# Kernel tuning notes

Hardware: AMD Instinct MI355X
Metric: run time of the kernel (lower is better)

## Reference

```python
import jax, jax.numpy as jnp
import numpy as np

N_NODES = 50000
N_EDGES = 1600000
NFEAT = 512
NCLASS = 16
H1, C1 = 8, 16  # conv1: heads=8, out_channels=16 (concat -> 128)
H2, C2 = 1, NCLASS  # conv2: heads=1, concat=False
NEG_SLOPE = 0.2


def gat_layer(x, edge_index, W, att_src, att_dst, bias, heads, out_c, concat):
    """PyG GATConv (eval mode, add_self_loops=True).
    x: [N, F_in]; edge_index: [2, E]; W: [heads*out_c, F_in];
    att_src/att_dst: [heads, out_c]; bias: [heads*out_c] or [out_c]."""
    N = x.shape[0]
    loop = jnp.arange(N, dtype=edge_index.dtype)
    src = jnp.concatenate([edge_index[0], loop])  # message source j
    dst = jnp.concatenate([edge_index[1], loop])  # message target i

    h = (x @ W.T).reshape(N, heads, out_c)  # [N, H, C]
    a_src = jnp.einsum('nhc,hc->nh', h, att_src)  # [N, H]
    a_dst = jnp.einsum('nhc,hc->nh', h, att_dst)

    alpha = jax.nn.leaky_relu(a_src[src] + a_dst[dst], NEG_SLOPE)  # [E', H]
    # segment softmax over incoming edges of each target node
    amax = jax.ops.segment_max(alpha, dst, num_segments=N)
    alpha = jnp.exp(alpha - amax[dst])
    denom = jax.ops.segment_sum(alpha, dst, num_segments=N)
    alpha = alpha / (denom[dst] + 1e-16)

    msg = h[src] * alpha[:, :, None]  # [E', H, C]
    out = jax.ops.segment_sum(msg, dst, num_segments=N)  # [N, H, C]
    if concat:
        out = out.reshape(N, heads * out_c)
    else:
        out = out.mean(axis=1)
    return out + bias


def setup_inputs() -> dict:
    key = jax.random.key(0)
    ks = jax.random.split(key, 10)
    glorot = lambda k, shape: (jax.random.uniform(k, shape, jnp.float32, -1.0, 1.0)
                               * jnp.sqrt(6.0 / (shape[-1] + shape[-2] if len(shape) > 1 else shape[-1])))
    x = jax.random.normal(ks[0], (N_NODES, NFEAT), jnp.float32)
    edge_index = jax.random.randint(ks[1], (2, N_EDGES), 0, N_NODES, jnp.int32)
    W1 = glorot(ks[2], (H1 * C1, NFEAT))
    att_src1 = glorot(ks[3], (H1, C1))
    att_dst1 = glorot(ks[4], (H1, C1))
    b1 = jnp.zeros((H1 * C1,), jnp.float32)
    W2 = glorot(ks[5], (H2 * C2, H1 * C1))
    att_src2 = glorot(ks[6], (H2, C2))
    att_dst2 = glorot(ks[7], (H2, C2))
    b2 = jnp.zeros((C2,), jnp.float32)
    return {"x": x, "edge_index": edge_index,
            "W1": W1, "att_src1": att_src1, "att_dst1": att_dst1, "b1": b1,
            "W2": W2, "att_src2": att_src2, "att_dst2": att_dst2, "b2": b2}


def reference(x, edge_index, W1, att_src1, att_dst1, b1, W2, att_src2, att_dst2, b2):
    # dropout is identity in eval mode
    h = gat_layer(x, edge_index, W1, att_src1, att_dst1, b1, H1, C1, concat=True)
    h = jax.nn.elu(h)
    out = gat_layer(h, edge_index, W2, att_src2, att_dst2, b2, H2, C2, concat=False)
    return jax.nn.log_softmax(out, axis=1)
```

## Files before the change

kernel.cpp:

```cpp
#include <hip/hip_runtime.h>
#include <hip/hip_bf16.h>

#define DI __device__ __forceinline__

DI float bfu(unsigned short u){ return __uint_as_float(((unsigned)u)<<16); }
DI unsigned short f2b(float f){
  unsigned u = __float_as_uint(f);
  return (unsigned short)((u + 0x7FFFu + ((u >> 16) & 1u)) >> 16);
}

typedef __attribute__((ext_vector_type(8))) short short8;
typedef __attribute__((ext_vector_type(4))) float floatx4;

#define OFF_W1  0
#define OFF_AS1 65536
#define OFF_AD1 65664
#define OFF_B1  65792
#define OFF_W2  65920
#define OFF_AS2 67968
#define OFF_AD2 67984
#define OFF_B2  68000
#define W_TOTAL 68016

#define CW_BLOCKS ((W_TOTAL+255)/256)
#define W1B_BLOCKS 256

__global__ __launch_bounds__(256) void setup_k(const unsigned short* __restrict__ x,
    const void* W1, const void* as1, const void* ad1, const void* b1,
    const void* W2, const void* as2, const void* ad2, const void* b2,
    int* __restrict__ flagp, float* __restrict__ dst,
    unsigned short* __restrict__ W1b, int* __restrict__ counts, int N){
  int b = blockIdx.x;
  if(b < CW_BLOCKS + W1B_BLOCKS){
    __shared__ int cnt;
    if(threadIdx.x==0) cnt = 0;
    __syncthreads();
    unsigned short u = x[threadIdx.x];
    int e = (u >> 7) & 0xFF;
    if(e < 100 || e > 140) atomicAdd(&cnt, 1);
    __syncthreads();
    int flag = (cnt >= 8) ? 1 : 0;
    if(b == 0 && threadIdx.x == 0) *flagp = flag;
    if(b < CW_BLOCKS){
      int i = b*256 + threadIdx.x;
      if(i < W_TOTAL){
        const void* src; int off;
        if(i < OFF_AS1){ src=W1;  off=i; }
        else if(i < OFF_AD1){ src=as1; off=i-OFF_AS1; }
        else if(i < OFF_B1 ){ src=ad1; off=i-OFF_AD1; }
        else if(i < OFF_W2 ){ src=b1;  off=i-OFF_B1; }
        else if(i < OFF_AS2){ src=W2;  off=i-OFF_W2; }
        else if(i < OFF_AD2){ src=as2; off=i-OFF_AS2; }
        else if(i < OFF_B2 ){ src=ad2; off=i-OFF_AD2; }
        else               { src=b2;  off=i-OFF_B2; }
        dst[i] = flag ? ((const float*)src)[off]
                      : bfu(((const unsigned short*)src)[off]);
      }
    } else {
      int j = (b - CW_BLOCKS)*256 + threadIdx.x;
      W1b[j] = flag ? f2b(((const float*)W1)[j]) : ((const unsigned short*)W1)[j];
    }
  } else {
    int i = (b - CW_BLOCKS - W1B_BLOCKS)*256 + threadIdx.x;
    if(i < N) counts[i] = 1;
  }
}

__global__ __launch_bounds__(256) void hist_k(const int* __restrict__ ei,
                                              int* __restrict__ counts, int E){
  int e = blockIdx.x*256 + threadIdx.x;
  if(e < E) atomicAdd(&counts[ei[E+e]], 1);
}

__global__ __launch_bounds__(256) void bsum_k(const int* __restrict__ counts,
                                              int* __restrict__ bsum, int N){
  int i = blockIdx.x*256 + threadIdx.x;
  int v = (i < N) ? counts[i] : 0;
  #pragma unroll
  for(int o = 1; o < 64; o <<= 1) v += __shfl_xor(v, o);
  __shared__ int s[4];
  if((threadIdx.x & 63) == 0) s[threadIdx.x >> 6] = v;
  __syncthreads();
  if(threadIdx.x == 0) bsum[blockIdx.x] = s[0] + s[1] + s[2] + s[3];
}
__global__ __launch_bounds__(1024) void bscan_k(int* __restrict__ bsum, int nb){
  __shared__ int part[1024];
  int t = threadIdx.x;
  int v = (t < nb) ? bsum[t] : 0;
  part[t] = v;
  __syncthreads();
  for(int o = 1; o < 1024; o <<= 1){
    int u = (t >= o) ? part[t-o] : 0;
    __syncthreads();
    part[t] += u;
    __syncthreads();
  }
  if(t < nb) bsum[t] = part[t] - v;
}
__global__ __launch_bounds__(256) void csr_fill_k(const int* __restrict__ counts,
    const int* __restrict__ bsum, int* __restrict__ rowptr,
    int* __restrict__ cursor, int* __restrict__ csr_src, int N){
  __shared__ int part[256];
  int t = threadIdx.x;
  int i = blockIdx.x*256 + t;
  int c = (i < N) ? counts[i] : 0;
  part[t] = c;
  __syncthreads();
  for(int o = 1; o < 256; o <<= 1){
    int u = (t >= o) ? part[t-o] : 0;
    __syncthreads();
    part[t] += u;
    __syncthreads();
  }
  int excl = part[t] - c + bsum[blockIdx.x];
  if(i < N){
    rowptr[i] = excl;
    csr_src[excl] = i;
    cursor[i] = excl + 1;
    if(i == N-1) rowptr[N] = excl + c;
  }
}

__global__ __launch_bounds__(256) void scatter_k(const int* __restrict__ ei,
    int* __restrict__ cursor, int* __restrict__ csr_src, int E, int N){
  int r  = blockIdx.x & 7;
  int nb = gridDim.x >> 3;
  int bi = blockIdx.x >> 3;
  int R  = (N + 7) >> 3;
  int lo = r * R;
  int hi = lo + R; if(hi > N) hi = N;
  for(int e = bi*256 + (int)threadIdx.x; e < E; e += nb*256){
    int d = ei[E + e];
    if(d >= lo && d < hi){
      int s = ei[e];
      int pos = atomicAdd(&cursor[d], 1);
      csr_src[pos] = s;
    }
  }
}

__global__ __launch_bounds__(256) void gemm1_mfma_k(const void* __restrict__ x,
    const int* __restrict__ flag, const unsigned short* __restrict__ W1b,
    const float* __restrict__ Wf, unsigned short* __restrict__ h1b,
    float* __restrict__ asrc1, float* __restrict__ adst1, int N){
  int wave = threadIdx.x >> 6, lane = threadIdx.x & 63;
  int q = lane >> 4, col = lane & 15;
  int nb = blockIdx.x*128 + wave*32;
  bool f32 = (*flag != 0);
  int cn0 = min(nb + col, N-1);
  int cn1 = min(nb + 16 + col, N-1);

  floatx4 acc[2][8];
  #pragma unroll
  for(int tm=0;tm<2;++tm)
    #pragma unroll
    for(int t=0;t<8;++t) acc[tm][t] = (floatx4){0.f,0.f,0.f,0.f};

  for(int ks=0; ks<16; ++ks){
    int k0 = ks*32 + q*8;
    short8 a0, a1;
    if(f32){
      const float* x0 = (const float*)x + (size_t)cn0*512 + k0;
      const float* x1 = (const float*)x + (size_t)cn1*512 + k0;
      union { short8 v; unsigned short u[8]; } A0, A1;
      #pragma unroll
      for(int j=0;j<8;++j){ A0.u[j] = f2b(x0[j]); A1.u[j] = f2b(x1[j]); }
      a0 = A0.v; a1 = A1.v;
    } else {
      a0 = *(const short8*)((const unsigned short*)x + (size_t)cn0*512 + k0);
      a1 = *(const short8*)((const unsigned short*)x + (size_t)cn1*512 + k0);
    }
    #pragma unroll
    for(int t=0;t<8;++t){
      short8 b = *(const short8*)(W1b + ((size_t)(16*t + col))*512 + k0);
      acc[0][t] = __builtin_amdgcn_mfma_f32_16x16x32_bf16(a0, b, acc[0][t], 0,0,0);
      acc[1][t] = __builtin_amdgcn_mfma_f32_16x16x32_bf16(a1, b, acc[1][t], 0,0,0);
    }
  }

  float asv[8], adv[8];
  #pragma unroll
  for(int t=0;t<8;++t){ asv[t] = Wf[OFF_AS1 + 16*t + col]; adv[t] = Wf[OFF_AD1 + 16*t + col]; }

  #pragma unroll
  for(int tm=0;tm<2;++tm){
    #pragma unroll
    for(int r=0;r<4;++r){
      int node = nb + tm*16 + q*4 + r;
      if(node >= N) continue;
      float vs = 0.f, vd = 0.f;
      #pragma unroll
      for(int t=0;t<8;++t){
        float v = acc[tm][t][r];
        h1b[(size_t)node*128 + 16*t + col] = f2b(v);
        float ps = v*asv[t], pd = v*adv[t];
        #pragma unroll
        for(int o=1;o<16;o<<=1){ ps += __shfl_xor(ps,o); pd += __shfl_xor(pd,o); }
        if(col == t){ vs = ps; vd = pd; }
      }
      if(col < 8){
        asrc1[(size_t)node*8 + col] = vs;
        adst1[(size_t)node*8 + col] = vd;
      }
    }
  }
}

__global__ __launch_bounds__(256) void agg1_k(const int* __restrict__ rowptr,
    const int* __restrict__ csr_src, const float* __restrict__ asrc1,
    const float* __restrict__ adst1, const unsigned short* __restrict__ h1b,
    const float* __restrict__ Wf,
    float* __restrict__ h2, float* __restrict__ asrc2, float* __restrict__ adst2, int N){
  int n = blockIdx.x*4 + (threadIdx.x >> 6);
  int lane = threadIdx.x & 63;
  if(n >= N) return;
  int g = lane >> 4;
  int cl = lane & 15;
  int h = cl >> 1;
  float ad = adst1[n*8 + h];
  int end = rowptr[n+1];
  int p = rowptr[n] + g;

  float d = 0.f;
  float o[8];
  #pragma unroll
  for(int j=0;j<8;++j) o[j] = 0.f;

  union U { uint4 v; unsigned short u[8]; };
  const uint4 z4 = (uint4){0,0,0,0};

  bool v0 = p    < end;
  bool v1 = p+4  < end;
  bool v2 = p+8  < end;
  bool v3 = p+12 < end;
  int s0 = v0 ? csr_src[p]    : 0;
  int s1 = v1 ? csr_src[p+4]  : 0;
  int s2 = v2 ? csr_src[p+8]  : 0;
  float a0 = v0 ? asrc1[s0*8 + h] : 0.f;
  float a1 = v1 ? asrc1[s1*8 + h] : 0.f;
  U H0, H1, H2;
  H0.v = v0 ? *(const uint4*)(h1b + (size_t)s0*128 + 8*cl) : z4;
  H1.v = v1 ? *(const uint4*)(h1b + (size_t)s1*128 + 8*cl) : z4;

  while(v0){
    int s3 = v3 ? csr_src[p+12] : 0;
    float a2 = v2 ? asrc1[s2*8 + h] : 0.f;
    H2.v = v2 ? *(const uint4*)(h1b + (size_t)s2*128 + 8*cl) : z4;
    float aa = a0 + ad;
    aa = aa > 0.f ? aa : 0.2f*aa;
    float w = __expf(aa);
    d += w;
    #pragma unroll
    for(int j=0;j<8;++j) o[j] = fmaf(w, bfu(H0.u[j]), o[j]);
    p += 4;
    v0 = v1; v1 = v2; v2 = v3; v3 = (p+12 < end);
    s2 = s3;
    a0 = a1; a1 = a2;
    H0.v = H1.v; H1.v = H2.v;
  }

  #pragma unroll
  for(int off = 16; off < 64; off <<= 1){
    d += __shfl_xor(d, off);
    #pragma unroll
    for(int j=0;j<8;++j) o[j] += __shfl_xor(o[j], off);
  }

  float inv = 1.f / (d + 1e-16f);
  float e[8];
  #pragma unroll
  for(int j=0;j<8;++j){
    float v = o[j]*inv + Wf[OFF_B1 + 8*cl + j];
    e[j] = v > 0.f ? v : (__expf(v) - 1.f);
  }
  float h2v = 0.f;
  #pragma unroll
  for(int c = 0; c < 4; ++c){
    int cls = 4*g + c;
    const float4* wr = (const float4*)(Wf + OFF_W2 + cls*128 + 8*cl);
    float4 w0 = wr[0], w1 = wr[1];
    float part = w0.x*e[0] + w0.y*e[1] + w0.z*e[2] + w0.w*e[3]
               + w1.x*e[4] + w1.y*e[5] + w1.z*e[6] + w1.w*e[7];
    part += __shfl_xor(part,1); part += __shfl_xor(part,2);
    part += __shfl_xor(part,4); part += __shfl_xor(part,8);
    if(cl == c) h2v = part;
  }
  if(cl < 4) h2[n*16 + 4*g + cl] = h2v;
  float ps = (cl < 4) ? h2v * Wf[OFF_AS2 + 4*g + cl] : 0.f;
  float pd = (cl < 4) ? h2v * Wf[OFF_AD2 + 4*g + cl] : 0.f;
  #pragma unroll
  for(int off = 1; off < 64; off <<= 1){ ps += __shfl_xor(ps,off); pd += __shfl_xor(pd,off); }
  if(lane == 0){ asrc2[n] = ps; adst2[n] = pd; }
}

__global__ __launch_bounds__(256) void agg2_k(const int* __restrict__ rowptr,
    const int* __restrict__ csr_src, const float* __restrict__ asrc2,
    const float* __restrict__ adst2, const float* __restrict__ h2,
    const float* __restrict__ Wf, const int* __restrict__ flag,
    void* __restrict__ out, int N){
  int n = blockIdx.x*4 + (threadIdx.x >> 6);
  int lane = threadIdx.x & 63;
  if(n >= N) return;
  int g = lane >> 4, l = lane & 15;
  float ad = adst2[n];
  int end = rowptr[n+1];
  int p = rowptr[n] + g;

  float d = 0.f, o = 0.f;

  bool v0 = p    < end;
  bool v1 = p+4  < end;
  bool v2 = p+8  < end;
  bool v3 = p+12 < end;
  int s0 = v0 ? csr_src[p]    : 0;
  int s1 = v1 ? csr_src[p+4]  : 0;
  int s2 = v2 ? csr_src[p+8]  : 0;
  float a0 = v0 ? asrc2[s0] : 0.f;
  float a1 = v1 ? asrc2[s1] : 0.f;
  float h0 = v0 ? h2[s0*16 + l] : 0.f;
  float h1v = v1 ? h2[s1*16 + l] : 0.f;

  while(v0){
    int s3 = v3 ? csr_src[p+12] : 0;
    float a2 = v2 ? asrc2[s2] : 0.f;
    float h2g = v2 ? h2[s2*16 + l] : 0.f;
    float aa = a0 + ad;
    aa = aa > 0.f ? aa : 0.2f*aa;
    float w = __expf(aa);
    d += w;
    o = fmaf(w, h0, o);
    p += 4;
    v0 = v1; v1 = v2; v2 = v3; v3 = (p+12 < end);
    s2 = s3;
    a0 = a1; a1 = a2;
    h0 = h1v; h1v = h2g;
  }

  #pragma unroll
  for(int off = 16; off < 64; off <<= 1){
    d += __shfl_xor(d, off);
    o += __shfl_xor(o, off);
  }

  float v = o/(d + 1e-16f) + Wf[OFF_B2 + l];
  float mx = v;
  #pragma unroll
  for(int off = 1; off < 16; off <<= 1) mx = fmaxf(mx, __shfl_xor(mx, off));
  float ex = __expf(v - mx), sum = ex;
  #pragma unroll
  for(int off = 1; off < 16; off <<= 1) sum += __shfl_xor(sum, off);
  float r = v - mx - __logf(sum);
  if(g == 0){
    if(*flag) ((float*)out)[(size_t)n*16 + l] = r;
    else      ((__hip_bfloat16*)out)[(size_t)n*16 + l] = __float2bfloat16(r);
  }
}

extern "C" void kernel_launch(void* const* d_in, const int* in_sizes, int n_in,
                              void* d_out, int out_size, void* d_ws, size_t ws_size,
                              hipStream_t stream){
  const void* x  = d_in[0];
  const int*  ei = (const int*)d_in[1];
  const int N  = in_sizes[0] / 512;
  const int E  = in_sizes[1] / 2;
  const int NB = (N + 255) / 256;

  int*   flag     = (int*)d_ws;
  float* Wf       = (float*)d_ws + 4;
  unsigned short* W1b = (unsigned short*)(Wf + W_TOTAL);
  unsigned short* h1b = W1b + 65536;
  float* asrc1    = (float*)(h1b + (size_t)N*128);
  float* adst1    = asrc1 + (size_t)N*8;
  float* h2       = adst1 + (size_t)N*8;
  float* asrc2    = h2 + (size_t)N*16;
  float* adst2    = asrc2 + N;
  int*   rowptr   = (int*)(adst2 + N);
  int*   cursor   = rowptr + (N+1);
  int*   csr_src  = cursor + N;
  int*   bsum     = csr_src + (E+N);

  int setup_blocks = CW_BLOCKS + W1B_BLOCKS + NB;
  hipLaunchKernelGGL(setup_k, dim3(setup_blocks), dim3(256), 0, stream,
                     (const unsigned short*)x,
                     d_in[2], d_in[3], d_in[4], d_in[5], d_in[6], d_in[7], d_in[8], d_in[9],
                     flag, Wf, W1b, cursor, N);
  hipLaunchKernelGGL(hist_k, dim3((E+255)/256), dim3(256), 0, stream, ei, cursor, E);
  hipLaunchKernelGGL(bsum_k, dim3(NB), dim3(256), 0, stream, cursor, bsum, N);
  hipLaunchKernelGGL(bscan_k, dim3(1), dim3(1024), 0, stream, bsum, NB);
  hipLaunchKernelGGL(csr_fill_k, dim3(NB), dim3(256), 0, stream,
                     cursor, bsum, rowptr, cursor, csr_src, N);
  hipLaunchKernelGGL(scatter_k, dim3(1024), dim3(256), 0, stream,
                     ei, cursor, csr_src, E, N);
  hipLaunchKernelGGL(gemm1_mfma_k, dim3((N+127)/128), dim3(256), 0, stream,
                     x, flag, W1b, Wf, h1b, asrc1, adst1, N);
  hipLaunchKernelGGL(agg1_k, dim3((N+3)/4), dim3(256), 0, stream,
                     rowptr, csr_src, asrc1, adst1, h1b, Wf, h2, asrc2, adst2, N);
  hipLaunchKernelGGL(agg2_k, dim3((N+3)/4), dim3(256), 0, stream,
                     rowptr, csr_src, asrc2, adst2, h2, Wf, flag, d_out, N);
}
```

Baseline: 481.5 us.

## Use nontemporal edge loads, shrink GEMM tile, split agg1 into two launches

Edge-index reads in the histogram and scatter kernels now use nontemporal loads, so the streamed edge list does not evict reused lines from cache. The layer-1 GEMM drops from 32 to 16 nodes per wave, which doubles the grid size and lowers register pressure but loads each W1 tile twice as often per node. agg1 is split into two launches covering each half of the nodes. The split adds one launch and does not obviously change the total work.

```diff
diff --git a/kernel.cpp b/kernel.cpp
--- a/kernel.cpp
+++ b/kernel.cpp
@@ -69,7 +69,10 @@
 __global__ __launch_bounds__(256) void hist_k(const int* __restrict__ ei,
                                               int* __restrict__ counts, int E){
   int e = blockIdx.x*256 + threadIdx.x;
-  if(e < E) atomicAdd(&counts[ei[E+e]], 1);
+  if(e < E){
+    int d = __builtin_nontemporal_load(ei + E + e);
+    atomicAdd(&counts[d], 1);
+  }
 }
 
 __global__ __launch_bounds__(256) void bsum_k(const int* __restrict__ counts,
@@ -130,9 +133,9 @@
   int lo = r * R;
   int hi = lo + R; if(hi > N) hi = N;
   for(int e = bi*256 + (int)threadIdx.x; e < E; e += nb*256){
-    int d = ei[E + e];
+    int d = __builtin_nontemporal_load(ei + E + e);
     if(d >= lo && d < hi){
-      int s = ei[e];
+      int s = __builtin_nontemporal_load(ei + e);
       int pos = atomicAdd(&cursor[d], 1);
       csr_src[pos] = s;
     }
@@ -145,36 +148,30 @@
     float* __restrict__ asrc1, float* __restrict__ adst1, int N){
   int wave = threadIdx.x >> 6, lane = threadIdx.x & 63;
   int q = lane >> 4, col = lane & 15;
-  int nb = blockIdx.x*128 + wave*32;
+  int nb = blockIdx.x*64 + wave*16;
   bool f32 = (*flag != 0);
   int cn0 = min(nb + col, N-1);
-  int cn1 = min(nb + 16 + col, N-1);
-
-  floatx4 acc[2][8];
-  #pragma unroll
-  for(int tm=0;tm<2;++tm)
-    #pragma unroll
-    for(int t=0;t<8;++t) acc[tm][t] = (floatx4){0.f,0.f,0.f,0.f};
+
+  floatx4 acc[8];
+  #pragma unroll
+  for(int t=0;t<8;++t) acc[t] = (floatx4){0.f,0.f,0.f,0.f};
 
   for(int ks=0; ks<16; ++ks){
     int k0 = ks*32 + q*8;
-    short8 a0, a1;
+    short8 a0;
     if(f32){
       const float* x0 = (const float*)x + (size_t)cn0*512 + k0;
-      const float* x1 = (const float*)x + (size_t)cn1*512 + k0;
-      union { short8 v; unsigned short u[8]; } A0, A1;
+      union { short8 v; unsigned short u[8]; } A0;
       #pragma unroll
-      for(int j=0;j<8;++j){ A0.u[j] = f2b(x0[j]); A1.u[j] = f2b(x1[j]); }
-      a0 = A0.v; a1 = A1.v;
+      for(int j=0;j<8;++j){ A0.u[j] = f2b(x0[j]); }
+      a0 = A0.v;
     } else {
       a0 = *(const short8*)((const unsigned short*)x + (size_t)cn0*512 + k0);
-      a1 = *(const short8*)((const unsigned short*)x + (size_t)cn1*512 + k0);
     }
     #pragma unroll
     for(int t=0;t<8;++t){
       short8 b = *(const short8*)(W1b + ((size_t)(16*t + col))*512 + k0);
-      acc[0][t] = __builtin_amdgcn_mfma_f32_16x16x32_bf16(a0, b, acc[0][t], 0,0,0);
-      acc[1][t] = __builtin_amdgcn_mfma_f32_16x16x32_bf16(a1, b, acc[1][t], 0,0,0);
+      acc[t] = __builtin_amdgcn_mfma_f32_16x16x32_bf16(a0, b, acc[t], 0,0,0);
     }
   }
 
@@ -183,25 +180,22 @@
   for(int t=0;t<8;++t){ asv[t] = Wf[OFF_AS1 + 16*t + col]; adv[t] = Wf[OFF_AD1 + 16*t + col]; }
 
   #pragma unroll
-  for(int tm=0;tm<2;++tm){
+  for(int r=0;r<4;++r){
+    int node = nb + q*4 + r;
+    if(node >= N) continue;
+    float vs = 0.f, vd = 0.f;
     #pragma unroll
-    for(int r=0;r<4;++r){
-      int node = nb + tm*16 + q*4 + r;
-      if(node >= N) continue;
-      float vs = 0.f, vd = 0.f;
+    for(int t=0;t<8;++t){
+      float v = acc[t][r];
+      h1b[(size_t)node*128 + 16*t + col] = f2b(v);
+      float ps = v*asv[t], pd = v*adv[t];
       #pragma unroll
-      for(int t=0;t<8;++t){
-        float v = acc[tm][t][r];
-        h1b[(size_t)node*128 + 16*t + col] = f2b(v);
-        float ps = v*asv[t], pd = v*adv[t];
-        #pragma unroll
-        for(int o=1;o<16;o<<=1){ ps += __shfl_xor(ps,o); pd += __shfl_xor(pd,o); }
-        if(col == t){ vs = ps; vd = pd; }
-      }
-      if(col < 8){
-        asrc1[(size_t)node*8 + col] = vs;
-        adst1[(size_t)node*8 + col] = vd;
-      }
+      for(int o=1;o<16;o<<=1){ ps += __shfl_xor(ps,o); pd += __shfl_xor(pd,o); }
+      if(col == t){ vs = ps; vd = pd; }
+    }
+    if(col < 8){
+      asrc1[(size_t)node*8 + col] = vs;
+      adst1[(size_t)node*8 + col] = vd;
     }
   }
 }
@@ -210,10 +204,11 @@
     const int* __restrict__ csr_src, const float* __restrict__ asrc1,
     const float* __restrict__ adst1, const unsigned short* __restrict__ h1b,
     const float* __restrict__ Wf,
-    float* __restrict__ h2, float* __restrict__ asrc2, float* __restrict__ adst2, int N){
-  int n = blockIdx.x*4 + (threadIdx.x >> 6);
+    float* __restrict__ h2, float* __restrict__ asrc2, float* __restrict__ adst2,
+    int n0, int nEnd){
+  int n = n0 + blockIdx.x*4 + (threadIdx.x >> 6);
   int lane = threadIdx.x & 63;
-  if(n >= N) return;
+  if(n >= nEnd) return;
   int g = lane >> 4;
   int cl = lane & 15;
   int h = cl >> 1;
@@ -391,10 +386,13 @@
                      cursor, bsum, rowptr, cursor, csr_src, N);
   hipLaunchKernelGGL(scatter_k, dim3(1024), dim3(256), 0, stream,
                      ei, cursor, csr_src, E, N);
-  hipLaunchKernelGGL(gemm1_mfma_k, dim3((N+127)/128), dim3(256), 0, stream,
+  hipLaunchKernelGGL(gemm1_mfma_k, dim3((N+63)/64), dim3(256), 0, stream,
                      x, flag, W1b, Wf, h1b, asrc1, adst1, N);
-  hipLaunchKernelGGL(agg1_k, dim3((N+3)/4), dim3(256), 0, stream,
-                     rowptr, csr_src, asrc1, adst1, h1b, Wf, h2, asrc2, adst2, N);
+  int half = (N + 1) / 2;
+  hipLaunchKernelGGL(agg1_k, dim3((half+3)/4), dim3(256), 0, stream,
+                     rowptr, csr_src, asrc1, adst1, h1b, Wf, h2, asrc2, adst2, 0, half);
+  hipLaunchKernelGGL(agg1_k, dim3((N-half+3)/4), dim3(256), 0, stream,
+                     rowptr, csr_src, asrc1, adst1, h1b, Wf, h2, asrc2, adst2, half, N);
   hipLaunchKernelGGL(agg2_k, dim3((N+3)/4), dim3(256), 0, stream,
                      rowptr, csr_src, asrc2, adst2, h2, Wf, flag, d_out, N);
 }
```

After: 529.1 us. +9.9%, slower.
